# Kernel optimization log

Measured on AMD Instinct MI355X. Metric: run time of the kernel, lower is better.

## Reference

```python
import jax, jax.numpy as jnp
import numpy as np

B, L, D, DIN, A, V, R = 1024, 100, 256, 704, 128, 32000, 129


def setup_inputs() -> dict:
    key = jax.random.key(0)
    ks = jax.random.split(key, 18)
    s = 0.05
    inp = {
        "x": jax.random.normal(ks[0], (B, DIN), jnp.float32),
        "h0": jax.random.normal(ks[1], (B, D), jnp.float32),
        "c0": jax.random.normal(ks[2], (B, D), jnp.float32),
        "src_enc": jax.random.normal(ks[3], (B, L, D), jnp.float32),
        "src_token_ids": jax.random.randint(ks[4], (B, L), 0, V),
        "W_ih": jax.random.normal(ks[5], (4 * D, DIN), jnp.float32) * s,
        "b_ih": jax.random.normal(ks[6], (4 * D,), jnp.float32) * s,
        "W_hh": jax.random.normal(ks[7], (4 * D, D), jnp.float32) * s,
        "b_hh": jax.random.normal(ks[8], (4 * D,), jnp.float32) * s,
        "W_attn": jax.random.normal(ks[9], (D, D), jnp.float32) * s,
        "W_att_vec": jax.random.normal(ks[10], (A * 2, 2 * D), jnp.float32) * s,
        "W_ptr": jax.random.normal(ks[11], (D, D), jnp.float32) * s,
        "rule_emb": jax.random.normal(ks[12], (R, 128), jnp.float32) * s,
        "W_rule_proj": jax.random.normal(ks[13], (D, 128), jnp.float32) * s,
        "prim_emb": jax.random.normal(ks[14], (V, 128), jnp.float32) * s,
        "W_prim_proj": jax.random.normal(ks[15], (D, 128), jnp.float32) * s,
        "w_gen": jax.random.normal(ks[16], (2, D), jnp.float32) * s,
        "b_gen": jax.random.normal(ks[17], (2,), jnp.float32) * s,
    }
    # W_att_vec maps concat(h, ctx) [2D] -> ATT (=256); keep shape (256, 512)
    inp["W_att_vec"] = inp["W_att_vec"][:256]
    return inp


def reference(x, h0, c0, src_enc, src_token_ids, W_ih, b_ih, W_hh, b_hh,
              W_attn, W_att_vec, W_ptr, rule_emb, W_rule_proj,
              prim_emb, W_prim_proj, w_gen, b_gen):
    # --- LSTMCell (torch gate order i, f, g, o) ---
    gates = x @ W_ih.T + b_ih + h0 @ W_hh.T + b_hh          # [B, 4D]
    i, f, g, o = jnp.split(gates, 4, axis=-1)
    i, f, o = jax.nn.sigmoid(i), jax.nn.sigmoid(f), jax.nn.sigmoid(o)
    c = f * c0 + i * jnp.tanh(g)
    h = o * jnp.tanh(c)                                      # [B, D]

    # --- dot-product attention over source encodings ---
    enc_proj = src_enc @ W_attn.T                            # [B, L, D]
    scores = jnp.einsum('bd,bld->bl', h, enc_proj)
    alpha = jax.nn.softmax(scores, axis=-1)
    ctx = jnp.einsum('bl,bld->bd', alpha, src_enc)
    att = jnp.tanh(jnp.concatenate([h, ctx], axis=-1) @ W_att_vec.T)  # [B, 256]

    # --- apply-rule (production) readout ---
    rule_proj = rule_emb @ W_rule_proj.T                     # [R, 256]
    log_p_rule = jax.nn.log_softmax(att @ rule_proj.T, axis=-1)  # [B, R]

    # --- primitive generation readout ---
    prim_proj = prim_emb @ W_prim_proj.T                     # [V, 256]
    p_gen_prim = jax.nn.softmax(att @ prim_proj.T, axis=-1)  # [B, V]

    # --- pointer network copy distribution over source positions ---
    ptr_scores = jnp.einsum('bld,bd->bl', src_enc @ W_ptr.T, att)
    copy_p = jax.nn.softmax(ptr_scores, axis=-1)             # [B, L]

    # --- gen vs copy gate (softmax over 2, per usage in parse()) ---
    gate = jax.nn.softmax(att @ w_gen.T + b_gen, axis=-1)    # [B, 2]

    # --- combined primitive distribution: gen + scattered copy mass ---
    p_prim = gate[:, :1] * p_gen_prim                        # [B, V]
    copy_mass = gate[:, 1:] * copy_p                         # [B, L]
    bidx = jnp.arange(p_prim.shape[0])[:, None]
    p_prim = p_prim.at[bidx, src_token_ids].add(copy_mass)
    return log_p_rule, p_prim, h, c, att
```

## Files before the change

kernel.cpp:

```cpp
#include <hip/hip_runtime.h>
#include <hip/hip_bf16.h>
#include <math.h>

#define NB   1024
#define LL   100
#define DD   256
#define DINN 704
#define VV   32000
#define RR   129
#define KAV  512
#define ROWU 129

typedef float f32x4 __attribute__((ext_vector_type(4)));
typedef float f32x2 __attribute__((ext_vector_type(2)));
typedef short s16x8 __attribute__((ext_vector_type(8)));
typedef unsigned short u16;
typedef unsigned int u32;

__device__ __forceinline__ float sigf(float x) { return 1.0f / (1.0f + __expf(-x)); }

__device__ __forceinline__ u16 f2bf(float f) {
    u32 u = __float_as_uint(f);
    u += 0x7fffu + ((u >> 16) & 1u);
    return (u16)(u >> 16);
}
__device__ __forceinline__ float bf2f(u16 s) {
    return __uint_as_float(((u32)s) << 16);
}

__global__ __launch_bounds__(256) void k_lstm(
    const float* __restrict__ x, const float* __restrict__ h0, const float* __restrict__ c0,
    const float* __restrict__ W_ih, const float* __restrict__ b_ih,
    const float* __restrict__ W_hh, const float* __restrict__ b_hh,
    float* __restrict__ out_h, float* __restrict__ out_c)
{
    __shared__ __align__(16) float As[16][36];
    __shared__ __align__(16) float Bs[16][68];
    __shared__ __align__(16) float gsm[32][68];
    const int t = threadIdx.x;
    const int row0 = blockIdx.x * 32;
    const int dg = blockIdx.y;
    const int tr = t >> 4, tc = t & 15;
    float acc[2][4] = {};

    for (int kt = 0; kt < 60; ++kt) {
        const float* __restrict__ Asrc;
        const float* __restrict__ Bsrc;
        int lda, kb;
        if (kt < 44) { Asrc = x;  Bsrc = W_ih; lda = DINN; kb = kt * 16; }
        else         { Asrc = h0; Bsrc = W_hh; lda = DD;   kb = (kt - 44) * 16; }
        __syncthreads();
#pragma unroll
        for (int p = 0; p < 2; ++p) {
            int e = t + p * 256;
            int r = e >> 4, kk = e & 15;
            As[kk][r] = Asrc[(row0 + r) * lda + kb + kk];
        }
#pragma unroll
        for (int p = 0; p < 4; ++p) {
            int e = t + p * 256;
            int r = e >> 4, kk = e & 15;
            int n = ((r >> 4) << 8) + dg * 16 + (r & 15);
            Bs[kk][r] = Bsrc[n * lda + kb + kk];
        }
        __syncthreads();
#pragma unroll
        for (int kk = 0; kk < 16; ++kk) {
            float a0 = As[kk][tr * 2], a1 = As[kk][tr * 2 + 1];
            f32x4 b = *reinterpret_cast<const f32x4*>(&Bs[kk][tc * 4]);
#pragma unroll
            for (int i = 0; i < 4; ++i) {
                acc[0][i] = fmaf(a0, b[i], acc[0][i]);
                acc[1][i] = fmaf(a1, b[i], acc[1][i]);
            }
        }
    }
    __syncthreads();
#pragma unroll
    for (int j = 0; j < 2; ++j)
#pragma unroll
        for (int i = 0; i < 4; ++i)
            gsm[tr * 2 + j][tc * 4 + i] = acc[j][i];
    __syncthreads();

#pragma unroll
    for (int p = 0; p < 2; ++p) {
        int item = t + p * 256;
        int r = item >> 4, di = item & 15;
        int dcol = dg * 16 + di;
        float iv = gsm[r][di]      + b_ih[dcol]          + b_hh[dcol];
        float fv = gsm[r][16 + di] + b_ih[DD + dcol]     + b_hh[DD + dcol];
        float gv = gsm[r][32 + di] + b_ih[2 * DD + dcol] + b_hh[2 * DD + dcol];
        float ov = gsm[r][48 + di] + b_ih[3 * DD + dcol] + b_hh[3 * DD + dcol];
        float cprev = c0[(row0 + r) * DD + dcol];
        float cc = sigf(fv) * cprev + sigf(iv) * tanhf(gv);
        float hh = sigf(ov) * tanhf(cc);
        out_c[(row0 + r) * DD + dcol] = cc;
        out_h[(row0 + r) * DD + dcol] = hh;
    }
}

__global__ __launch_bounds__(256) void k_conv(
    const float* __restrict__ src, u16* __restrict__ dst,
    const float* __restrict__ rule_emb, const float* __restrict__ W_rule_proj,
    float* __restrict__ rule_proj)
{
    __shared__ float re_s[128];
    const int bx = blockIdx.x, t = threadIdx.x;

    if (bx < RR && t < 128) re_s[t] = rule_emb[bx * 128 + t];

    int i = (bx * 256 + t) * 8;
    f32x4 a = *reinterpret_cast<const f32x4*>(&src[i]);
    f32x4 b = *reinterpret_cast<const f32x4*>(&src[i + 4]);
    s16x8 r;
    r[0] = (short)f2bf(a[0]); r[1] = (short)f2bf(a[1]);
    r[2] = (short)f2bf(a[2]); r[3] = (short)f2bf(a[3]);
    r[4] = (short)f2bf(b[0]); r[5] = (short)f2bf(b[1]);
    r[6] = (short)f2bf(b[2]); r[7] = (short)f2bf(b[3]);
    *reinterpret_cast<s16x8*>(&dst[i]) = r;

    if (bx < RR) {
        __syncthreads();
        float acc = 0.f;
        const float* __restrict__ wr = &W_rule_proj[t * 128];
#pragma unroll 8
        for (int k = 0; k < 128; k += 4) {
            f32x4 w4 = *reinterpret_cast<const f32x4*>(&wr[k]);
            acc += w4[0] * re_s[k] + w4[1] * re_s[k + 1]
                 + w4[2] * re_s[k + 2] + w4[3] * re_s[k + 3];
        }
        rule_proj[bx * DD + t] = acc;
    }
}

__global__ __launch_bounds__(256) void k_hw(
    const float* __restrict__ h, const float* __restrict__ W_attn, float* __restrict__ hW)
{
    __shared__ __align__(16) float As[16][36];
    __shared__ __align__(16) float Bs[16][68];
    const int t = threadIdx.x;
    const int row0 = blockIdx.x * 32;
    const int col0 = blockIdx.y * 64;
    const int tr = t >> 4, tc = t & 15;
    float acc[2][4] = {};
    for (int kt = 0; kt < 16; ++kt) {
        __syncthreads();
#pragma unroll
        for (int p = 0; p < 2; ++p) {
            int e = t + p * 256;
            int r = e >> 4, kk = e & 15;
            As[kk][r] = h[(row0 + r) * DD + kt * 16 + kk];
        }
#pragma unroll
        for (int p = 0; p < 4; ++p) {
            int e = t + p * 256;
            int kk = e >> 6, c = e & 63;
            Bs[kk][c] = W_attn[(kt * 16 + kk) * DD + col0 + c];
        }
        __syncthreads();
#pragma unroll
        for (int kk = 0; kk < 16; ++kk) {
            float a0 = As[kk][tr * 2], a1 = As[kk][tr * 2 + 1];
            f32x4 b = *reinterpret_cast<const f32x4*>(&Bs[kk][tc * 4]);
#pragma unroll
            for (int i = 0; i < 4; ++i) {
                acc[0][i] = fmaf(a0, b[i], acc[0][i]);
                acc[1][i] = fmaf(a1, b[i], acc[1][i]);
            }
        }
    }
#pragma unroll
    for (int j = 0; j < 2; ++j) {
        f32x4 v;
#pragma unroll
        for (int i = 0; i < 4; ++i) v[i] = acc[j][i];
        *reinterpret_cast<f32x4*>(&hW[(row0 + tr * 2 + j) * DD + col0 + tc * 4]) = v;
    }
}

__global__ __launch_bounds__(256) void k_attn2(
    const float* __restrict__ src_enc, const float* __restrict__ hW,
    float* __restrict__ ctx_out)
{
    __shared__ u32 enc_u[LL * ROWU];
    __shared__ __align__(16) float part[4][DD];
    __shared__ __align__(16) float hw_s[DD];
    __shared__ float sc_s[LL];
    __shared__ float al_s[LL];

    const int b = blockIdx.x, t = threadIdx.x;
    const int lane = t & 63, w = t >> 6;
    const float* __restrict__ enc = src_enc + (size_t)b * LL * DD;

    hw_s[t] = hW[b * DD + t];

#pragma unroll 5
    for (int p = 0; p < 25; ++p) {
        int q = p * 256 + t;
        int l = q >> 6, dq = q & 63;
        f32x4 ev = *reinterpret_cast<const f32x4*>(&enc[l * DD + dq * 4]);
        u32 w0 = (u32)f2bf(ev[0]) | ((u32)f2bf(ev[1]) << 16);
        u32 w1 = (u32)f2bf(ev[2]) | ((u32)f2bf(ev[3]) << 16);
        enc_u[l * ROWU + dq * 2]     = w0;
        enc_u[l * ROWU + dq * 2 + 1] = w1;
    }
    __syncthreads();

    {
        const int sl = ((w >> 1) << 6) + lane;
        float sp = 0.f;
        if (sl < LL) {
            const u32* __restrict__ rp = enc_u + sl * ROWU + ((w & 1) << 6);
            const float* __restrict__ hp = hw_s + ((w & 1) << 7);
#pragma unroll 16
            for (int k = 0; k < 64; ++k) {
                u32 v = rp[k];
                sp = fmaf(bf2f((u16)v),         hp[2 * k],     sp);
                sp = fmaf(bf2f((u16)(v >> 16)), hp[2 * k + 1], sp);
            }
        }
        part[w][lane] = sp;
    }
    __syncthreads();
    if (t < LL) sc_s[t] = part[(t >> 6) << 1][t & 63] + part[((t >> 6) << 1) + 1][t & 63];
    __syncthreads();

    if (w == 0) {
        float v0 = sc_s[lane];
        float v1 = (lane + 64 < LL) ? sc_s[lane + 64] : -1e30f;
        float m = fmaxf(v0, v1);
#pragma unroll
        for (int s = 1; s < 64; s <<= 1) m = fmaxf(m, __shfl_xor(m, s));
        float e0 = __expf(v0 - m);
        float e1 = (lane + 64 < LL) ? __expf(v1 - m) : 0.f;
        float ssum = e0 + e1;
#pragma unroll
        for (int s = 1; s < 64; s <<= 1) ssum += __shfl_xor(ssum, s);
        float inv = 1.f / ssum;
        al_s[lane] = e0 * inv;
        if (lane + 64 < LL) al_s[lane + 64] = e1 * inv;
    }
    __syncthreads();

    {
        const int l0 = w * 25;
        float c0 = 0.f, c1 = 0.f, c2 = 0.f, c3 = 0.f;
#pragma unroll 5
        for (int li = 0; li < 25; ++li) {
            int l = l0 + li;
            float a = al_s[l];
            u32 v0 = enc_u[l * ROWU + lane * 2];
            u32 v1 = enc_u[l * ROWU + lane * 2 + 1];
            c0 = fmaf(a, bf2f((u16)v0), c0);
            c1 = fmaf(a, bf2f((u16)(v0 >> 16)), c1);
            c2 = fmaf(a, bf2f((u16)v1), c2);
            c3 = fmaf(a, bf2f((u16)(v1 >> 16)), c3);
        }
        f32x4 p; p[0] = c0; p[1] = c1; p[2] = c2; p[3] = c3;
        *reinterpret_cast<f32x4*>(&part[w][lane * 4]) = p;
    }
    __syncthreads();
    ctx_out[b * DD + t] = (part[0][t] + part[1][t]) + (part[2][t] + part[3][t]);
}

__global__ __launch_bounds__(256) void k_att(
    const float* __restrict__ h, const float* __restrict__ ctx,
    const float* __restrict__ W_att_vec, float* __restrict__ att_out)
{
    __shared__ __align__(16) float As[16][36];
    __shared__ __align__(16) float Bs[16][68];
    const int t = threadIdx.x;
    const int row0 = blockIdx.x * 32;
    const int col0 = blockIdx.y * 64;
    const int tr = t >> 4, tc = t & 15;
    float acc[2][4] = {};
    for (int kt = 0; kt < 32; ++kt) {
        const float* __restrict__ Asrc = (kt < 16) ? h : ctx;
        int kb = (kt < 16) ? kt * 16 : (kt - 16) * 16;
        int kg = kt * 16;
        __syncthreads();
#pragma unroll
        for (int p = 0; p < 2; ++p) {
            int e = t + p * 256;
            int r = e >> 4, kk = e & 15;
            As[kk][r] = Asrc[(row0 + r) * DD + kb + kk];
        }
#pragma unroll
        for (int p = 0; p < 4; ++p) {
            int e = t + p * 256;
            int r = e >> 4, kk = e & 15;
            Bs[kk][r] = W_att_vec[(col0 + r) * KAV + kg + kk];
        }
        __syncthreads();
#pragma unroll
        for (int kk = 0; kk < 16; ++kk) {
            float a0 = As[kk][tr * 2], a1 = As[kk][tr * 2 + 1];
            f32x4 b = *reinterpret_cast<const f32x4*>(&Bs[kk][tc * 4]);
#pragma unroll
            for (int i = 0; i < 4; ++i) {
                acc[0][i] = fmaf(a0, b[i], acc[0][i]);
                acc[1][i] = fmaf(a1, b[i], acc[1][i]);
            }
        }
    }
#pragma unroll
    for (int j = 0; j < 2; ++j)
#pragma unroll
        for (int i = 0; i < 4; ++i)
            att_out[(row0 + tr * 2 + j) * DD + col0 + tc * 4 + i] = tanhf(acc[j][i]);
}

__global__ __launch_bounds__(256) void k_ptrproj(
    const float* __restrict__ att, const float* __restrict__ W_ptr,
    const float* __restrict__ W_prim_proj,
    float* __restrict__ atw, u16* __restrict__ att_bf)
{
    __shared__ __align__(16) float As[16][36];
    __shared__ __align__(16) float Bs[16][68];
    const int t = threadIdx.x;
    const int row0 = blockIdx.x * 32;
    const int col0 = blockIdx.y * 64;
    const int tr = t >> 4, tc = t & 15;
    float acc[2][4] = {};
    for (int kt = 0; kt < 16; ++kt) {
        __syncthreads();
#pragma unroll
        for (int p = 0; p < 2; ++p) {
            int e = t + p * 256;
            int r = e >> 4, kk = e & 15;
            As[kk][r] = att[(row0 + r) * DD + kt * 16 + kk];
        }
#pragma unroll
        for (int p = 0; p < 4; ++p) {
            int e = t + p * 256;
            int kk = e >> 6, c = e & 63;
            Bs[kk][c] = (col0 < 256)
                ? W_ptr[(kt * 16 + kk) * DD + col0 + c]
                : W_prim_proj[(kt * 16 + kk) * 128 + (col0 - 256) + c];
        }
        __syncthreads();
#pragma unroll
        for (int kk = 0; kk < 16; ++kk) {
            float a0 = As[kk][tr * 2], a1 = As[kk][tr * 2 + 1];
            f32x4 b = *reinterpret_cast<const f32x4*>(&Bs[kk][tc * 4]);
#pragma unroll
            for (int i = 0; i < 4; ++i) {
                acc[0][i] = fmaf(a0, b[i], acc[0][i]);
                acc[1][i] = fmaf(a1, b[i], acc[1][i]);
            }
        }
    }
    if (col0 < 256) {
#pragma unroll
        for (int j = 0; j < 2; ++j) {
            f32x4 v;
#pragma unroll
            for (int i = 0; i < 4; ++i) v[i] = acc[j][i];
            *reinterpret_cast<f32x4*>(&atw[(row0 + tr * 2 + j) * DD + col0 + tc * 4]) = v;
        }
    } else {
#pragma unroll
        for (int j = 0; j < 2; ++j)
#pragma unroll
            for (int i = 0; i < 4; ++i)
                att_bf[(row0 + tr * 2 + j) * 128 + (col0 - 256) + tc * 4 + i] = f2bf(acc[j][i]);
    }
}

__global__ __launch_bounds__(256) void k_rulegate(
    const float* __restrict__ att, const float* __restrict__ rule_proj,
    const float* __restrict__ w_gen, const float* __restrict__ b_gen,
    float* __restrict__ log_p_rule, float* __restrict__ gate0_ws,
    float* __restrict__ gate1_ws)
{
    __shared__ __align__(16) float att_s[DD];
    __shared__ float red_s[RR];
    __shared__ float gl_s[2];
    __shared__ float mS[2];
    const int b = blockIdx.x, t = threadIdx.x;
    const int lane = t & 63, w = t >> 6;
    att_s[t] = att[b * DD + t];
    __syncthreads();

    if (t < RR) {
        float acc = 0.f;
        const float* __restrict__ rp = &rule_proj[t * DD];
#pragma unroll 4
        for (int d = 0; d < DD; d += 4) {
            f32x4 r4 = *reinterpret_cast<const f32x4*>(&rp[d]);
            f32x4 a4 = *reinterpret_cast<const f32x4*>(&att_s[d]);
            acc += r4[0] * a4[0] + r4[1] * a4[1] + r4[2] * a4[2] + r4[3] * a4[3];
        }
        red_s[t] = acc;
    }
    if (w < 2) {
        f32x4 a4 = *reinterpret_cast<const f32x4*>(&att_s[lane * 4]);
        f32x4 g4 = *reinterpret_cast<const f32x4*>(&w_gen[w * DD + lane * 4]);
        float p = a4[0] * g4[0] + a4[1] * g4[1] + a4[2] * g4[2] + a4[3] * g4[3];
#pragma unroll
        for (int s = 1; s < 64; s <<= 1) p += __shfl_xor(p, s);
        if (lane == 0) gl_s[w] = p + b_gen[w];
    }
    __syncthreads();

    if (w == 0) {
        float v0 = red_s[lane];
        float v1 = red_s[lane + 64];
        float v2 = (lane == 0) ? red_s[128] : -1e30f;
        float m = fmaxf(fmaxf(v0, v1), v2);
#pragma unroll
        for (int s = 1; s < 64; s <<= 1) m = fmaxf(m, __shfl_xor(m, s));
        float ssum = __expf(v0 - m) + __expf(v1 - m) + ((lane == 0) ? __expf(v2 - m) : 0.f);
#pragma unroll
        for (int s = 1; s < 64; s <<= 1) ssum += __shfl_xor(ssum, s);
        if (lane == 0) { mS[0] = m; mS[1] = logf(ssum); }
    }
    __syncthreads();
    if (t < RR) log_p_rule[b * RR + t] = red_s[t] - mS[0] - mS[1];

    if (t == 0) {
        float g0 = gl_s[0], g1 = gl_s[1];
        float gm = fmaxf(g0, g1);
        float e0g = __expf(g0 - gm), e1g = __expf(g1 - gm);
        gate0_ws[b] = e0g / (e0g + e1g);
        gate1_ws[b] = e1g / (e0g + e1g);
    }
}

__global__ __launch_bounds__(256) void k_ptr2(
    const float* __restrict__ src_enc, const float* __restrict__ atw,
    const float* __restrict__ gate1_ws, float* __restrict__ copy_mass)
{
    __shared__ float sc_s[LL];
    const int b = blockIdx.x, t = threadIdx.x;
    const int lane = t & 63, w = t >> 6;
    const float* __restrict__ enc = src_enc + (size_t)b * LL * DD;
    f32x4 aw4 = *reinterpret_cast<const f32x4*>(&atw[b * DD + lane * 4]);

    for (int l = w; l < LL; l += 4) {
        f32x4 ev = *reinterpret_cast<const f32x4*>(&enc[l * DD + lane * 4]);
        float pr = aw4[0] * ev[0] + aw4[1] * ev[1] + aw4[2] * ev[2] + aw4[3] * ev[3];
#pragma unroll
        for (int m = 1; m < 64; m <<= 1) pr += __shfl_xor(pr, m);
        if (lane == 0) sc_s[l] = pr;
    }
    __syncthreads();
    if (w == 0) {
        float gate1 = gate1_ws[b];
        float v0 = sc_s[lane];
        float v1 = (lane + 64 < LL) ? sc_s[lane + 64] : -1e30f;
        float m = fmaxf(v0, v1);
#pragma unroll
        for (int s = 1; s < 64; s <<= 1) m = fmaxf(m, __shfl_xor(m, s));
        float ee0 = __expf(v0 - m);
        float ee1 = (lane + 64 < LL) ? __expf(v1 - m) : 0.f;
        float ssum = ee0 + ee1;
#pragma unroll
        for (int s = 1; s < 64; s <<= 1) ssum += __shfl_xor(ssum, s);
        float inv = 1.f / ssum;
        copy_mass[b * LL + lane] = gate1 * ee0 * inv;
        if (lane + 64 < LL) copy_mass[b * LL + lane + 64] = gate1 * ee1 * inv;
    }
}

template <int PASS>
__global__ __launch_bounds__(256) void k_prim(
    const u16* __restrict__ att_bf, const u16* __restrict__ prim_bf,
    const float* __restrict__ coef, float* __restrict__ stats, float* __restrict__ p_prim)
{
    const int t = threadIdx.x;
    const int lane = t & 63, w = t >> 6;
    const int lm = lane & 15, lq = lane >> 4;
    const int colbase = blockIdx.x * 128 + (w & 1) * 64;
    const int chunk = colbase >> 6;
    const int rowblk = blockIdx.y * 256;

    s16x8 pfr[4][4];
#pragma unroll
    for (int kg = 0; kg < 4; ++kg)
#pragma unroll
        for (int mg = 0; mg < 4; ++mg)
            pfr[kg][mg] = *reinterpret_cast<const s16x8*>(
                &prim_bf[(size_t)(colbase + mg * 16 + lm) * 128 + kg * 32 + lq * 8]);

    for (int it = 0; it < 2; ++it) {
        const int rowbase = rowblk + it * 128 + (w >> 1) * 64;
        f32x4 acc[4][4] = {};
#pragma unroll
        for (int kg = 0; kg < 4; ++kg) {
            s16x8 afr[4];
#pragma unroll
            for (int ng = 0; ng < 4; ++ng)
                afr[ng] = *reinterpret_cast<const s16x8*>(
                    &att_bf[(rowbase + ng * 16 + lm) * 128 + kg * 32 + lq * 8]);
#pragma unroll
            for (int mg = 0; mg < 4; ++mg)
#pragma unroll
                for (int ng = 0; ng < 4; ++ng)
                    acc[mg][ng] = __builtin_amdgcn_mfma_f32_16x16x32_bf16(
                        pfr[kg][mg], afr[ng], acc[mg][ng], 0, 0, 0);
        }
        if (PASS == 0) {
#pragma unroll
            for (int ng = 0; ng < 4; ++ng) {
                float se = 0.f;
#pragma unroll
                for (int mg = 0; mg < 4; ++mg)
                    se += __expf(acc[mg][ng][0]) + __expf(acc[mg][ng][1])
                        + __expf(acc[mg][ng][2]) + __expf(acc[mg][ng][3]);
                se += __shfl_xor(se, 16);
                se += __shfl_xor(se, 32);
                if (lq == 0)
                    stats[chunk * NB + rowbase + ng * 16 + lm] = se;
            }
        } else {
#pragma unroll
            for (int ng = 0; ng < 4; ++ng) {
                const int arow = rowbase + ng * 16 + lm;
                const float cf = coef[arow];
                float* __restrict__ dst = &p_prim[(size_t)arow * VV + colbase + lq * 4];
#pragma unroll
                for (int mg = 0; mg < 4; ++mg) {
                    f32x4 v;
                    v[0] = cf * __expf(acc[mg][ng][0]);
                    v[1] = cf * __expf(acc[mg][ng][1]);
                    v[2] = cf * __expf(acc[mg][ng][2]);
                    v[3] = cf * __expf(acc[mg][ng][3]);
                    *reinterpret_cast<f32x4*>(&dst[mg * 16]) = v;
                }
            }
        }
    }
}

__global__ __launch_bounds__(256) void k_combine(
    const float* __restrict__ stats, const float* __restrict__ gate0_ws,
    float* __restrict__ coef)
{
    const int row = blockIdx.x * 256 + threadIdx.x;
    float s0 = 0.f, s1 = 0.f, s2 = 0.f, s3 = 0.f;
    for (int c = 0; c < 500; c += 4) {
        s0 += stats[(c)     * NB + row];
        s1 += stats[(c + 1) * NB + row];
        s2 += stats[(c + 2) * NB + row];
        s3 += stats[(c + 3) * NB + row];
    }
    coef[row] = gate0_ws[row] / ((s0 + s1) + (s2 + s3));
}

__global__ __launch_bounds__(256) void k_scatter(
    const int* __restrict__ tok, const float* __restrict__ copy_mass, float* __restrict__ p_prim)
{
    int i = blockIdx.x * 256 + threadIdx.x;
    if (i >= NB * LL) return;
    int b = i / LL;
    atomicAdd(&p_prim[(size_t)b * VV + tok[i]], copy_mass[i]);
}

extern "C" void kernel_launch(void* const* d_in, const int* in_sizes, int n_in,
                              void* d_out, int out_size, void* d_ws, size_t ws_size,
                              hipStream_t stream)
{
    const float* x         = (const float*)d_in[0];
    const float* h0        = (const float*)d_in[1];
    const float* c0        = (const float*)d_in[2];
    const float* src_enc   = (const float*)d_in[3];
    const int*   tok       = (const int*)  d_in[4];
    const float* W_ih      = (const float*)d_in[5];
    const float* b_ih      = (const float*)d_in[6];
    const float* W_hh      = (const float*)d_in[7];
    const float* b_hh      = (const float*)d_in[8];
    const float* W_attn    = (const float*)d_in[9];
    const float* W_att_vec = (const float*)d_in[10];
    const float* W_ptr     = (const float*)d_in[11];
    const float* rule_emb  = (const float*)d_in[12];
    const float* W_rule_pr = (const float*)d_in[13];
    const float* prim_emb  = (const float*)d_in[14];
    const float* W_prim_pr = (const float*)d_in[15];
    const float* w_gen     = (const float*)d_in[16];
    const float* b_gen     = (const float*)d_in[17];

    float* out    = (float*)d_out;
    float* o_logp = out;
    float* o_pp   = out + 1024 * 129;
    float* o_h    = o_pp + (size_t)1024 * 32000;
    float* o_c    = o_h + 1024 * 256;
    float* o_att  = o_c + 1024 * 256;

    float* wsf      = (float*)d_ws;
    float* ws_rp    = wsf;
    float* ws_gate0 = ws_rp    + 33280;
    float* ws_gate1 = ws_gate0 + 1024;
    float* ws_cm    = ws_gate1 + 1024;
    float* ws_coef  = ws_cm    + 102400;
    float* ws_hw    = ws_coef  + 1024;
    float* ws_ctx   = ws_hw    + 262144;
    float* ws_atw   = ws_ctx   + 262144;
    float* ws_stats = ws_atw   + 262144;
    u16*   ws_attbf = (u16*)(ws_stats + 512000);
    u16*   ws_primbf= (u16*)(ws_stats + 512000 + 65536);

    k_conv<<<dim3(2000), 256, 0, stream>>>(prim_emb, ws_primbf, rule_emb, W_rule_pr, ws_rp);
    k_lstm<<<dim3(32, 16), 256, 0, stream>>>(x, h0, c0, W_ih, b_ih, W_hh, b_hh, o_h, o_c);
    k_hw<<<dim3(32, 4), 256, 0, stream>>>(o_h, W_attn, ws_hw);
    k_attn2<<<dim3(1024), 256, 0, stream>>>(src_enc, ws_hw, ws_ctx);
    k_att<<<dim3(32, 4), 256, 0, stream>>>(o_h, ws_ctx, W_att_vec, o_att);
    k_ptrproj<<<dim3(32, 6), 256, 0, stream>>>(o_att, W_ptr, W_prim_pr, ws_atw, ws_attbf);
    k_rulegate<<<dim3(1024), 256, 0, stream>>>(o_att, ws_rp, w_gen, b_gen,
                                               o_logp, ws_gate0, ws_gate1);
    k_ptr2<<<dim3(1024), 256, 0, stream>>>(src_enc, ws_atw, ws_gate1, ws_cm);
    k_prim<0><<<dim3(250, 4), 256, 0, stream>>>(ws_attbf, ws_primbf, nullptr, ws_stats, nullptr);
    k_combine<<<dim3(4), 256, 0, stream>>>(ws_stats, ws_gate0, ws_coef);
    k_prim<1><<<dim3(250, 4), 256, 0, stream>>>(ws_attbf, ws_primbf, ws_coef, nullptr, o_pp);
    k_scatter<<<dim3(400), 256, 0, stream>>>(tok, ws_cm, o_pp);
}
```

Measured before the change: 259.4 us.

## Fold rule logits into ptrproj GEMM, lighten rule/gate kernel, retune ptr2 and attn

After: 257.7 us. No clear change (-0.7%).

```diff
diff --git a/kernel.cpp b/kernel.cpp
--- a/kernel.cpp
+++ b/kernel.cpp
@@ -28,7 +28,7 @@
     return __uint_as_float(((u32)s) << 16);
 }
 
-__global__ __launch_bounds__(256) void k_lstm(
+__global__ __launch_bounds__(256, 2) void k_lstm(
     const float* __restrict__ x, const float* __restrict__ h0, const float* __restrict__ c0,
     const float* __restrict__ W_ih, const float* __restrict__ b_ih,
     const float* __restrict__ W_hh, const float* __restrict__ b_hh,
@@ -103,7 +103,7 @@
 __global__ __launch_bounds__(256) void k_conv(
     const float* __restrict__ src, u16* __restrict__ dst,
     const float* __restrict__ rule_emb, const float* __restrict__ W_rule_proj,
-    float* __restrict__ rule_proj)
+    float* __restrict__ rpT)
 {
     __shared__ float re_s[128];
     const int bx = blockIdx.x, t = threadIdx.x;
@@ -130,7 +130,7 @@
             acc += w4[0] * re_s[k] + w4[1] * re_s[k + 1]
                  + w4[2] * re_s[k + 2] + w4[3] * re_s[k + 3];
         }
-        rule_proj[bx * DD + t] = acc;
+        rpT[t * 192 + bx] = acc;
     }
 }
 
@@ -179,7 +179,7 @@
     }
 }
 
-__global__ __launch_bounds__(256) void k_attn2(
+__global__ __launch_bounds__(256, 2) void k_attn2(
     const float* __restrict__ src_enc, const float* __restrict__ hW,
     float* __restrict__ ctx_out)
 {
@@ -195,7 +195,7 @@
 
     hw_s[t] = hW[b * DD + t];
 
-#pragma unroll 5
+#pragma unroll
     for (int p = 0; p < 25; ++p) {
         int q = p * 256 + t;
         int l = q >> 6, dq = q & 63;
@@ -213,7 +213,7 @@
         if (sl < LL) {
             const u32* __restrict__ rp = enc_u + sl * ROWU + ((w & 1) << 6);
             const float* __restrict__ hp = hw_s + ((w & 1) << 7);
-#pragma unroll 16
+#pragma unroll 32
             for (int k = 0; k < 64; ++k) {
                 u32 v = rp[k];
                 sp = fmaf(bf2f((u16)v),         hp[2 * k],     sp);
@@ -246,7 +246,7 @@
     {
         const int l0 = w * 25;
         float c0 = 0.f, c1 = 0.f, c2 = 0.f, c3 = 0.f;
-#pragma unroll 5
+#pragma unroll
         for (int li = 0; li < 25; ++li) {
             int l = l0 + li;
             float a = al_s[l];
@@ -313,8 +313,8 @@
 
 __global__ __launch_bounds__(256) void k_ptrproj(
     const float* __restrict__ att, const float* __restrict__ W_ptr,
-    const float* __restrict__ W_prim_proj,
-    float* __restrict__ atw, u16* __restrict__ att_bf)
+    const float* __restrict__ W_prim_proj, const float* __restrict__ rpT,
+    float* __restrict__ atw, u16* __restrict__ att_bf, float* __restrict__ rl)
 {
     __shared__ __align__(16) float As[16][36];
     __shared__ __align__(16) float Bs[16][68];
@@ -335,9 +335,14 @@
         for (int p = 0; p < 4; ++p) {
             int e = t + p * 256;
             int kk = e >> 6, c = e & 63;
-            Bs[kk][c] = (col0 < 256)
-                ? W_ptr[(kt * 16 + kk) * DD + col0 + c]
-                : W_prim_proj[(kt * 16 + kk) * 128 + (col0 - 256) + c];
+            float bv;
+            if (col0 < 256)      bv = W_ptr[(kt * 16 + kk) * DD + col0 + c];
+            else if (col0 < 384) bv = W_prim_proj[(kt * 16 + kk) * 128 + (col0 - 256) + c];
+            else {
+                int rc = col0 - 384 + c;
+                bv = (rc < RR) ? rpT[(kt * 16 + kk) * 192 + rc] : 0.f;
+            }
+            Bs[kk][c] = bv;
         }
         __syncthreads();
 #pragma unroll
@@ -359,93 +364,90 @@
             for (int i = 0; i < 4; ++i) v[i] = acc[j][i];
             *reinterpret_cast<f32x4*>(&atw[(row0 + tr * 2 + j) * DD + col0 + tc * 4]) = v;
         }
-    } else {
+    } else if (col0 < 384) {
 #pragma unroll
         for (int j = 0; j < 2; ++j)
 #pragma unroll
             for (int i = 0; i < 4; ++i)
                 att_bf[(row0 + tr * 2 + j) * 128 + (col0 - 256) + tc * 4 + i] = f2bf(acc[j][i]);
-    }
-}
-
-__global__ __launch_bounds__(256) void k_rulegate(
-    const float* __restrict__ att, const float* __restrict__ rule_proj,
+    } else {
+#pragma unroll
+        for (int j = 0; j < 2; ++j)
+#pragma unroll
+            for (int i = 0; i < 4; ++i) {
+                int rc = col0 - 384 + tc * 4 + i;
+                if (rc < RR) rl[(row0 + tr * 2 + j) * 132 + rc] = acc[j][i];
+            }
+    }
+}
+
+__global__ __launch_bounds__(256) void k_fin(
+    const float* __restrict__ rl, const float* __restrict__ att,
     const float* __restrict__ w_gen, const float* __restrict__ b_gen,
     float* __restrict__ log_p_rule, float* __restrict__ gate0_ws,
     float* __restrict__ gate1_ws)
 {
-    __shared__ __align__(16) float att_s[DD];
-    __shared__ float red_s[RR];
-    __shared__ float gl_s[2];
-    __shared__ float mS[2];
-    const int b = blockIdx.x, t = threadIdx.x;
-    const int lane = t & 63, w = t >> 6;
-    att_s[t] = att[b * DD + t];
-    __syncthreads();
-
-    if (t < RR) {
-        float acc = 0.f;
-        const float* __restrict__ rp = &rule_proj[t * DD];
-#pragma unroll 4
-        for (int d = 0; d < DD; d += 4) {
-            f32x4 r4 = *reinterpret_cast<const f32x4*>(&rp[d]);
-            f32x4 a4 = *reinterpret_cast<const f32x4*>(&att_s[d]);
-            acc += r4[0] * a4[0] + r4[1] * a4[1] + r4[2] * a4[2] + r4[3] * a4[3];
-        }
-        red_s[t] = acc;
-    }
-    if (w < 2) {
-        f32x4 a4 = *reinterpret_cast<const f32x4*>(&att_s[lane * 4]);
-        f32x4 g4 = *reinterpret_cast<const f32x4*>(&w_gen[w * DD + lane * 4]);
-        float p = a4[0] * g4[0] + a4[1] * g4[1] + a4[2] * g4[2] + a4[3] * g4[3];
-#pragma unroll
-        for (int s = 1; s < 64; s <<= 1) p += __shfl_xor(p, s);
-        if (lane == 0) gl_s[w] = p + b_gen[w];
-    }
-    __syncthreads();
-
-    if (w == 0) {
-        float v0 = red_s[lane];
-        float v1 = red_s[lane + 64];
-        float v2 = (lane == 0) ? red_s[128] : -1e30f;
-        float m = fmaxf(fmaxf(v0, v1), v2);
-#pragma unroll
-        for (int s = 1; s < 64; s <<= 1) m = fmaxf(m, __shfl_xor(m, s));
-        float ssum = __expf(v0 - m) + __expf(v1 - m) + ((lane == 0) ? __expf(v2 - m) : 0.f);
-#pragma unroll
-        for (int s = 1; s < 64; s <<= 1) ssum += __shfl_xor(ssum, s);
-        if (lane == 0) { mS[0] = m; mS[1] = logf(ssum); }
-    }
-    __syncthreads();
-    if (t < RR) log_p_rule[b * RR + t] = red_s[t] - mS[0] - mS[1];
-
-    if (t == 0) {
-        float g0 = gl_s[0], g1 = gl_s[1];
-        float gm = fmaxf(g0, g1);
-        float e0g = __expf(g0 - gm), e1g = __expf(g1 - gm);
-        gate0_ws[b] = e0g / (e0g + e1g);
-        gate1_ws[b] = e1g / (e0g + e1g);
-    }
-}
-
-__global__ __launch_bounds__(256) void k_ptr2(
+    const int w = threadIdx.x >> 6, lane = threadIdx.x & 63;
+    const int b = blockIdx.x * 4 + w;
+
+    float v0 = rl[b * 132 + lane];
+    float v1 = rl[b * 132 + 64 + lane];
+    float v2 = (lane == 0) ? rl[b * 132 + 128] : -1e30f;
+    float m = fmaxf(fmaxf(v0, v1), v2);
+#pragma unroll
+    for (int s = 1; s < 64; s <<= 1) m = fmaxf(m, __shfl_xor(m, s));
+    float ssum = __expf(v0 - m) + __expf(v1 - m) + ((lane == 0) ? __expf(v2 - m) : 0.f);
+#pragma unroll
+    for (int s = 1; s < 64; s <<= 1) ssum += __shfl_xor(ssum, s);
+    float ls = m + logf(ssum);
+    log_p_rule[b * RR + lane] = v0 - ls;
+    log_p_rule[b * RR + 64 + lane] = v1 - ls;
+    if (lane == 0) log_p_rule[b * RR + 128] = v2 - ls;
+
+    f32x4 a4 = *reinterpret_cast<const f32x4*>(&att[b * DD + lane * 4]);
+    f32x4 g0 = *reinterpret_cast<const f32x4*>(&w_gen[lane * 4]);
+    f32x4 g1 = *reinterpret_cast<const f32x4*>(&w_gen[DD + lane * 4]);
+    float p0 = a4[0] * g0[0] + a4[1] * g0[1] + a4[2] * g0[2] + a4[3] * g0[3];
+    float p1 = a4[0] * g1[0] + a4[1] * g1[1] + a4[2] * g1[2] + a4[3] * g1[3];
+#pragma unroll
+    for (int s = 1; s < 64; s <<= 1) { p0 += __shfl_xor(p0, s); p1 += __shfl_xor(p1, s); }
+    if (lane == 0) {
+        float ga = p0 + b_gen[0], gb = p1 + b_gen[1];
+        float gm = fmaxf(ga, gb);
+        float ea = __expf(ga - gm), eb = __expf(gb - gm);
+        gate0_ws[b] = ea / (ea + eb);
+        gate1_ws[b] = eb / (ea + eb);
+    }
+}
+
+__global__ __launch_bounds__(256, 4) void k_ptr2(
     const float* __restrict__ src_enc, const float* __restrict__ atw,
     const float* __restrict__ gate1_ws, float* __restrict__ copy_mass)
 {
+    __shared__ __align__(16) float aw_s[DD];
     __shared__ float sc_s[LL];
     const int b = blockIdx.x, t = threadIdx.x;
     const int lane = t & 63, w = t >> 6;
-    const float* __restrict__ enc = src_enc + (size_t)b * LL * DD;
-    f32x4 aw4 = *reinterpret_cast<const f32x4*>(&atw[b * DD + lane * 4]);
-
-    for (int l = w; l < LL; l += 4) {
-        f32x4 ev = *reinterpret_cast<const f32x4*>(&enc[l * DD + lane * 4]);
-        float pr = aw4[0] * ev[0] + aw4[1] * ev[1] + aw4[2] * ev[2] + aw4[3] * ev[3];
-#pragma unroll
-        for (int m = 1; m < 64; m <<= 1) pr += __shfl_xor(pr, m);
-        if (lane == 0) sc_s[l] = pr;
-    }
-    __syncthreads();
+
+    aw_s[t] = atw[b * DD + t];
+    __syncthreads();
+
+    if (t < LL) {
+        const float* __restrict__ er = src_enc + (size_t)b * LL * DD + t * DD;
+        float a0 = 0.f, a1 = 0.f, a2 = 0.f, a3 = 0.f;
+#pragma unroll 16
+        for (int d = 0; d < 64; ++d) {
+            f32x4 ev = *reinterpret_cast<const f32x4*>(&er[d * 4]);
+            f32x4 av = *reinterpret_cast<const f32x4*>(&aw_s[d * 4]);
+            a0 = fmaf(ev[0], av[0], a0);
+            a1 = fmaf(ev[1], av[1], a1);
+            a2 = fmaf(ev[2], av[2], a2);
+            a3 = fmaf(ev[3], av[3], a3);
+        }
+        sc_s[t] = (a0 + a1) + (a2 + a3);
+    }
+    __syncthreads();
+
     if (w == 0) {
         float gate1 = gate1_ws[b];
         float v0 = sc_s[lane];
@@ -589,8 +591,9 @@
     float* o_att  = o_c + 1024 * 256;
 
     float* wsf      = (float*)d_ws;
-    float* ws_rp    = wsf;
-    float* ws_gate0 = ws_rp    + 33280;
+    float* ws_rpT   = wsf;
+    float* ws_rl    = ws_rpT   + 49152;
+    float* ws_gate0 = ws_rl    + 135168;
     float* ws_gate1 = ws_gate0 + 1024;
     float* ws_cm    = ws_gate1 + 1024;
     float* ws_coef  = ws_cm    + 102400;
@@ -601,14 +604,15 @@
     u16*   ws_attbf = (u16*)(ws_stats + 512000);
     u16*   ws_primbf= (u16*)(ws_stats + 512000 + 65536);
 
-    k_conv<<<dim3(2000), 256, 0, stream>>>(prim_emb, ws_primbf, rule_emb, W_rule_pr, ws_rp);
+    k_conv<<<dim3(2000), 256, 0, stream>>>(prim_emb, ws_primbf, rule_emb, W_rule_pr, ws_rpT);
     k_lstm<<<dim3(32, 16), 256, 0, stream>>>(x, h0, c0, W_ih, b_ih, W_hh, b_hh, o_h, o_c);
     k_hw<<<dim3(32, 4), 256, 0, stream>>>(o_h, W_attn, ws_hw);
     k_attn2<<<dim3(1024), 256, 0, stream>>>(src_enc, ws_hw, ws_ctx);
     k_att<<<dim3(32, 4), 256, 0, stream>>>(o_h, ws_ctx, W_att_vec, o_att);
-    k_ptrproj<<<dim3(32, 6), 256, 0, stream>>>(o_att, W_ptr, W_prim_pr, ws_atw, ws_attbf);
-    k_rulegate<<<dim3(1024), 256, 0, stream>>>(o_att, ws_rp, w_gen, b_gen,
-                                               o_logp, ws_gate0, ws_gate1);
+    k_ptrproj<<<dim3(32, 9), 256, 0, stream>>>(o_att, W_ptr, W_prim_pr, ws_rpT,
+                                               ws_atw, ws_attbf, ws_rl);
+    k_fin<<<dim3(256), 256, 0, stream>>>(ws_rl, o_att, w_gen, b_gen,
+                                         o_logp, ws_gate0, ws_gate1);
     k_ptr2<<<dim3(1024), 256, 0, stream>>>(src_enc, ws_atw, ws_gate1, ws_cm);
     k_prim<0><<<dim3(250, 4), 256, 0, stream>>>(ws_attbf, ws_primbf, nullptr, ws_stats, nullptr);
     k_combine<<<dim3(4), 256, 0, stream>>>(ws_stats, ws_gate0, ws_coef);
```
